# Kernel tuning notes

Hardware: AMD Instinct MI355X
Metric: run time of the kernel (lower is better)

Reference implementation:

```python
import jax, jax.numpy as jnp
import numpy as np

B, S, D, H = 2, 2048, 1024, 16
DH = D // H


def setup_inputs() -> dict:
    key = jax.random.key(0)
    ks = jax.random.split(key, 6)
    scale = 0.02
    X = jax.random.normal(ks[0], (B, S, D), dtype=jnp.float32)
    masks = jax.random.randint(ks[1], (B, S), 0, 2).astype(jnp.int32)
    Wq = jax.random.normal(ks[2], (D, D), dtype=jnp.float32) * scale
    Wk = jax.random.normal(ks[3], (D, D), dtype=jnp.float32) * scale
    Wv = jax.random.normal(ks[4], (D, D), dtype=jnp.float32) * scale
    Wo = jax.random.normal(ks[5], (D, D), dtype=jnp.float32) * scale
    return {"X": X, "masks": masks, "Wq": Wq, "Wk": Wk, "Wv": Wv, "Wo": Wo}


def reference(X, masks, Wq, Wk, Wv, Wo):
    b, s, d = X.shape
    masks_b = masks.astype(bool)                       # [B,S] key validity
    lookahead = jnp.triu(jnp.ones((s, s), dtype=bool), 1)  # [S,S] future positions
    pad = ~masks_b[:, None, :]                         # [B,1,S] -> invalid keys
    invalid = pad | lookahead[None, :, :]              # [B,S,S]
    valid = (~invalid)[:, None, :, :].astype(X.dtype)  # [B,1,S,S]

    def split_heads(Y):  # [B,S,D] -> [B,H,S,DH]
        return Y.reshape(b, s, H, DH).transpose(0, 2, 1, 3)

    Q = split_heads(X @ Wq.T)
    K = split_heads(X @ Wk.T)
    V = split_heads(X @ Wv.T)

    Qn = Q / jnp.sqrt(jnp.sum(Q * Q, axis=-1, keepdims=True))
    Kn = K / jnp.sqrt(jnp.sum(K * K, axis=-1, keepdims=True))

    scores = jnp.einsum('bhqd,bhkd->bhqk', Qn, Kn)     # cosine similarities
    att = jax.nn.relu(scores) * valid                  # relu + causal/pad mask
    ctx = jnp.einsum('bhqk,bhkd->bhqd', att, V)
    ctx = ctx * masks_b[:, None, :, None].astype(X.dtype)  # zero padded queries

    out = ctx.transpose(0, 2, 1, 3).reshape(b, s, d)
    return out @ Wo.T
```

## Files before the change

### kernel.cpp

```cpp
#include <hip/hip_runtime.h>
#include <hip/hip_bf16.h>

#define BB 2
#define SS 2048
#define DD 1024
#define HH 16
#define MMR (BB*SS)
#define ND3 3072

typedef __hip_bfloat16 bf;
typedef __bf16 bf16x8 __attribute__((ext_vector_type(8)));
typedef float f32x4 __attribute__((ext_vector_type(4)));
typedef float f32x16 __attribute__((ext_vector_type(16)));

#define VMCNT(n) asm volatile("s_waitcnt vmcnt(" #n ")" ::: "memory")

__device__ __forceinline__ f32x4 mfma16(bf16x8 a, bf16x8 b, f32x4 c) {
    return __builtin_amdgcn_mfma_f32_16x16x32_bf16(a, b, c, 0, 0, 0);
}
__device__ __forceinline__ f32x16 mfma32(bf16x8 a, bf16x8 b, f32x16 c) {
    return __builtin_amdgcn_mfma_f32_32x32x16_bf16(a, b, c, 0, 0, 0);
}
__device__ __forceinline__ unsigned cvt_pk_bf16(float lo, float hi) {
    unsigned r;
    asm("v_cvt_pk_bf16_f32 %0, %1, %2" : "=v"(r) : "v"(lo), "v"(hi));
    return r;
}
__device__ __forceinline__ void pl32swap(unsigned& a, unsigned& b) {
    asm("v_permlane32_swap_b32 %0, %1" : "+v"(a), "+v"(b));
}
__device__ __forceinline__ void glds16(const bf* g, bf* l) {
    __builtin_amdgcn_global_load_lds(
        (const __attribute__((address_space(1))) void*)g,
        (__attribute__((address_space(3))) void*)l,
        16, 0, 0);
}

__global__ __launch_bounds__(256) void k_convert(const float* __restrict__ X,
                                                 const float* __restrict__ Wq,
                                                 const float* __restrict__ Wk,
                                                 const float* __restrict__ Wv,
                                                 const float* __restrict__ Wo,
                                                 bf* __restrict__ Xb,
                                                 bf* __restrict__ Wqkv,
                                                 bf* __restrict__ Wob) {
    const int bid = blockIdx.x;
    const float* src;
    bf* dst;
    int off;
    if (bid < 4096) {
        src = X; dst = Xb; off = bid;
    } else {
        const int r = (bid - 4096) >> 10;
        src = (r == 0) ? Wq : (r == 1) ? Wk : (r == 2) ? Wv : Wo;
        dst = (r < 3) ? (Wqkv + (size_t)r * 1048576) : Wob;
        off = (bid - 4096) & 1023;
    }
    const int j = (off * 256 + threadIdx.x) * 4;
    float4 v = *(const float4*)(src + j);
    bf tmp[4];
    tmp[0] = __float2bfloat16(v.x);
    tmp[1] = __float2bfloat16(v.y);
    tmp[2] = __float2bfloat16(v.z);
    tmp[3] = __float2bfloat16(v.w);
    *(uint2*)(dst + j) = *(const uint2*)tmp;
}

__global__ __launch_bounds__(512, 6) void k_gemm8(const bf* __restrict__ A,
                                                  const bf* __restrict__ Bt,
                                                  const int* __restrict__ masks,
                                                  bf* __restrict__ Qn,
                                                  bf* __restrict__ Kn,
                                                  bf* __restrict__ Vt,
                                                  int nx, int K) {
    __shared__ __align__(16) bf Asm[3][128 * 32];
    __shared__ __align__(16) bf Bsm[3][128 * 32];
    const int tid = threadIdx.x;
    const int w = tid >> 6, lane = tid & 63, g = lane >> 4, rl = lane & 15;
    const int cpx = gridDim.x >> 3;
    const int swz = (blockIdx.x & 7) * cpx + (blockIdx.x >> 3);
    const int m0 = (swz / nx) * 128, n0 = (swz % nx) * 128;
    const int wr = (w >> 1) * 32, wc = (w & 1) * 64;
    const int lrow = lane >> 2, lseg = lane & 3;
    const int xseg = lseg ^ ((lrow >> 1) & 3);

    f32x4 acc[2][4] = {};
    const bf* Ap = A + (size_t)m0 * K;
    const bf* Bp = Bt + (size_t)n0 * K;

    auto stage = [&](int bi, int k0) {
        glds16(Ap + (size_t)(w * 16 + lrow) * K + k0 + xseg * 8, &Asm[bi][w * 512]);
        glds16(Bp + (size_t)(w * 16 + lrow) * K + k0 + xseg * 8, &Bsm[bi][w * 512]);
    };

    const int T = K >> 5;
    stage(0, 0);
    stage(1, 32);
    int cur = 0, nxt = 2;
    for (int t = 0; t < T; ++t) {
        __builtin_amdgcn_sched_barrier(0);
        if (t < T - 1) { VMCNT(2); } else { VMCNT(0); }
        __builtin_amdgcn_s_barrier();
        __builtin_amdgcn_sched_barrier(0);
        if (t + 2 < T) stage(nxt, (t + 2) * 32);

        const bf* Ab = Asm[cur];
        const bf* Bb = Bsm[cur];
        bf16x8 af[2], bfr[4];
#pragma unroll
        for (int m = 0; m < 2; ++m) {
            const int row = wr + m * 16 + rl;
            af[m] = __builtin_bit_cast(bf16x8,
                *(const int4*)&Ab[row * 32 + (g ^ ((row >> 1) & 3)) * 8]);
        }
#pragma unroll
        for (int n = 0; n < 4; ++n) {
            const int row = wc + n * 16 + rl;
            bfr[n] = __builtin_bit_cast(bf16x8,
                *(const int4*)&Bb[row * 32 + (g ^ ((row >> 1) & 3)) * 8]);
        }
        __builtin_amdgcn_s_setprio(1);
#pragma unroll
        for (int m = 0; m < 2; ++m)
#pragma unroll
            for (int n = 0; n < 4; ++n)
                acc[m][n] = mfma16(af[m], bfr[n], acc[m][n]);
        __builtin_amdgcn_s_setprio(0);

        cur = (cur == 2) ? 0 : cur + 1;
        nxt = (nxt == 2) ? 0 : nxt + 1;
    }

    const int ncol0 = n0 + wc;
    if (ncol0 < 2048) {
        bf* dst = (ncol0 < 1024) ? Qn : Kn;
        const int h2 = (ncol0 >> 6) & 15;
#pragma unroll
        for (int m = 0; m < 2; ++m) {
#pragma unroll
            for (int ri = 0; ri < 4; ++ri) {
                const int row = m0 + wr + m * 16 + g * 4 + ri;
                float ss = 0.f;
#pragma unroll
                for (int n = 0; n < 4; ++n) ss += acc[m][n][ri] * acc[m][n][ri];
#pragma unroll
                for (int d = 1; d < 16; d <<= 1) ss += __shfl_xor(ss, d, 64);
                const float sc = rsqrtf(ss) * (masks[row] ? 1.0f : 0.0f);
                const int b = row >> 11, s = row & 2047;
                const size_t base = ((size_t)(b * HH + h2) * SS + s) * 64;
#pragma unroll
                for (int n = 0; n < 4; ++n)
                    dst[base + n * 16 + rl] = __float2bfloat16(acc[m][n][ri] * sc);
            }
        }
    } else {
        const int h2 = (ncol0 - 2048) >> 6;
        const int b = (m0 + wr) >> 11;
        const int sb = ((m0 + wr) & 2047) + g * 4;
#pragma unroll
        for (int m = 0; m < 2; ++m)
#pragma unroll
            for (int n = 0; n < 4; ++n) {
                const int d = n * 16 + rl;
                bf t4[4];
#pragma unroll
                for (int ri = 0; ri < 4; ++ri) t4[ri] = __float2bfloat16(acc[m][n][ri]);
                *(uint2*)&Vt[((size_t)(b * HH + h2) * 64 + d) * SS + sb + m * 16] =
                    *(uint2*)t4;
            }
    }
}

__global__ __launch_bounds__(256) void k_gemm(const bf* __restrict__ A,
                                              const bf* __restrict__ Bt,
                                              float* __restrict__ Cf,
                                              int nx, int N, int K) {
    constexpr int BM = 64, BN = 128;
    __shared__ __align__(16) bf Asm[3][BM * 32];
    __shared__ __align__(16) bf Bsm[3][BN * 32];
    const int tid = threadIdx.x;
    const int w = tid >> 6, lane = tid & 63, g = lane >> 4, rl = lane & 15;
    const int cpx = gridDim.x >> 3;
    const int swz = (blockIdx.x & 7) * cpx + (blockIdx.x >> 3);
    const int m0 = (swz / nx) * BM, n0 = (swz % nx) * BN;
    const int wr = (w >> 1) * 32, wc = (w & 1) * 64;
    const int lrow = lane >> 2, lseg = lane & 3;
    const int xseg = lseg ^ ((lrow >> 1) & 3);

    f32x4 acc[2][4] = {};
    const bf* Ap = A + (size_t)m0 * K;
    const bf* Bp = Bt + (size_t)n0 * K;

    auto stage = [&](int bi, int k0) {
        glds16(Ap + (size_t)(w * 16 + lrow) * K + k0 + xseg * 8, &Asm[bi][w * 512]);
#pragma unroll
        for (int u = 0; u < 2; ++u)
            glds16(Bp + (size_t)(u * 64 + w * 16 + lrow) * K + k0 + xseg * 8,
                   &Bsm[bi][(u * 64 + w * 16) * 32]);
    };

    const int T = K >> 5;
    stage(0, 0);
    stage(1, 32);
    int cur = 0, nxt = 2;
    for (int t = 0; t < T; ++t) {
        __builtin_amdgcn_sched_barrier(0);
        if (t < T - 1) { VMCNT(3); } else { VMCNT(0); }
        __builtin_amdgcn_s_barrier();
        __builtin_amdgcn_sched_barrier(0);
        if (t + 2 < T) stage(nxt, (t + 2) * 32);

        const bf* Ab = Asm[cur];
        const bf* Bb = Bsm[cur];
        bf16x8 af[2], bfr[4];
#pragma unroll
        for (int m = 0; m < 2; ++m) {
            const int row = wr + m * 16 + rl;
            af[m] = __builtin_bit_cast(bf16x8,
                *(const int4*)&Ab[row * 32 + (g ^ ((row >> 1) & 3)) * 8]);
        }
#pragma unroll
        for (int n = 0; n < 4; ++n) {
            const int row = wc + n * 16 + rl;
            bfr[n] = __builtin_bit_cast(bf16x8,
                *(const int4*)&Bb[row * 32 + (g ^ ((row >> 1) & 3)) * 8]);
        }
        __builtin_amdgcn_s_setprio(1);
#pragma unroll
        for (int m = 0; m < 2; ++m)
#pragma unroll
            for (int n = 0; n < 4; ++n)
                acc[m][n] = mfma16(af[m], bfr[n], acc[m][n]);
        __builtin_amdgcn_s_setprio(0);

        cur = (cur == 2) ? 0 : cur + 1;
        nxt = (nxt == 2) ? 0 : nxt + 1;
    }

#pragma unroll
    for (int m = 0; m < 2; ++m)
#pragma unroll
        for (int n = 0; n < 4; ++n)
#pragma unroll
            for (int ri = 0; ri < 4; ++ri)
                Cf[(size_t)(m0 + wr + m * 16 + g * 4 + ri) * N + n0 + wc + n * 16 + rl] =
                    acc[m][n][ri];
}

__global__ __launch_bounds__(256) void k_attn(const bf* __restrict__ Qn,
                                              const bf* __restrict__ Kn,
                                              const bf* __restrict__ Vt,
                                              bf* __restrict__ Ctx) {
    __shared__ __align__(16) bf Ksm[2][64 * 64];
    __shared__ __align__(16) bf Vsm[2][64 * 64];

    const int idx = blockIdx.x;
    const int qt = 31 - (idx >> 5);
    const int by = idx & 31;
    const int b = by >> 4, h = by & 15;
    const int tid = threadIdx.x;
    const int w = tid >> 6, lane = tid & 63;
    const int l31 = lane & 31, hl = lane >> 5;
    const int qh = w >> 1;
    const int kp = w & 1;
    const int qw = qt * 64 + qh * 32;
    const int qg = qw + l31;

    const bf* Qp = Qn + (size_t)by * SS * 64;
    const bf* Kp = Kn + (size_t)by * SS * 64;
    const bf* Vp = Vt + (size_t)by * 64 * SS;

    bf16x8 aqs[4];
#pragma unroll
    for (int st = 0; st < 4; ++st)
        aqs[st] = __builtin_bit_cast(bf16x8,
            *(const int4*)(Qp + (size_t)(qw + l31) * 64 + st * 16 + hl * 8));

    const int srow = lane >> 3;
    const int sblk = (lane & 7) ^ srow;

    const bf* ksr = Kp + (size_t)(w * 16 + srow) * 64 + sblk * 8;
    const bf* vsr = Vp + (size_t)(w * 16 + srow) * SS + sblk * 8;
    bf* const kdst = &Ksm[0][w * 1024];
    bf* const vdst = &Vsm[0][w * 1024];

    auto stageP = [&](int buf, const bf* ks, const bf* vs) {
        glds16(ks,            kdst + buf * 4096);
        glds16(ks + 512,      kdst + buf * 4096 + 512);
        glds16(vs,            vdst + buf * 4096);
        glds16(vs + 8 * SS,   vdst + buf * 4096 + 512);
    };

    f32x16 accd[2] = {};

    auto doTile = [&](const bf* Ks, const bf* Vs, int t) {
        const int kb = t * 64 + kp * 32;
        if (kb > qw + 31) return;
        f32x16 pc = {};
        const int r = kp * 32 + l31;
#pragma unroll
        for (int st = 0; st < 4; ++st) {
            bf16x8 ak = __builtin_bit_cast(bf16x8,
                *(const int4*)&Ks[r * 64 + (((2 * st + hl) ^ (r & 7)) << 3)]);
            pc = mfma32(ak, aqs[st], pc);
        }
        const bool dg = (kb + 31 > qw);
        float pv[16];
#pragma unroll
        for (int m2 = 0; m2 < 16; ++m2) {
            float v = fmaxf(pc[m2], 0.0f);
            if (dg) {
                const int kg = kb + (m2 & 3) + 8 * (m2 >> 2) + 4 * hl;
                if (kg > qg) v = 0.0f;
            }
            pv[m2] = v;
        }
        unsigned P[8];
#pragma unroll
        for (int m2 = 0; m2 < 8; ++m2) P[m2] = cvt_pk_bf16(pv[2 * m2], pv[2 * m2 + 1]);
        pl32swap(P[0], P[2]);
        pl32swap(P[1], P[3]);
        pl32swap(P[4], P[6]);
        pl32swap(P[5], P[7]);
#pragma unroll
        for (int s = 0; s < 2; ++s) {
            uint4 pw = {P[4 * s + 0], P[4 * s + 1], P[4 * s + 2], P[4 * s + 3]};
            bf16x8 pa = __builtin_bit_cast(bf16x8, pw);
#pragma unroll
            for (int dt = 0; dt < 2; ++dt) {
                const int d = dt * 32 + l31;
                const int slot = kp * 4 + s * 2 + hl;
                bf16x8 bv = __builtin_bit_cast(bf16x8,
                    *(const int4*)&Vs[d * 64 + ((slot ^ (d & 7)) << 3)]);
                accd[dt] = mfma32(pa, bv, accd[dt]);
            }
        }
    };

    stageP(0, ksr, vsr);
    ksr += 4096; vsr += 64;
    __syncthreads();

    int t = 0;
    while (t + 1 <= qt) {
        stageP(1, ksr, vsr);
        ksr += 4096; vsr += 64;
        doTile(&Ksm[0][0], &Vsm[0][0], t);
        __syncthreads();
        if (t + 2 <= qt) {
            stageP(0, ksr, vsr);
            ksr += 4096; vsr += 64;
        }
        doTile(&Ksm[1][0], &Vsm[1][0], t + 1);
        __syncthreads();
        t += 2;
    }
    if (t <= qt) {
        doTile(&Ksm[0][0], &Vsm[0][0], t);
        __syncthreads();
    }

    float* red = (float*)&Ksm[0][0];
    if (kp == 1) {
#pragma unroll
        for (int dt = 0; dt < 2; ++dt)
#pragma unroll
            for (int m2 = 0; m2 < 16; ++m2)
                red[qh * 2048 + (dt * 16 + m2) * 64 + lane] = accd[dt][m2];
    }
    __syncthreads();
    if (kp == 0) {
#pragma unroll
        for (int dt = 0; dt < 2; ++dt)
#pragma unroll
            for (int m2 = 0; m2 < 16; ++m2) {
                const float v = accd[dt][m2] + red[qh * 2048 + (dt * 16 + m2) * 64 + lane];
                const int q = qw + (m2 & 3) + 8 * (m2 >> 2) + 4 * hl;
                const int d = dt * 32 + l31;
                Ctx[(size_t)(b * SS + q) * DD + h * 64 + d] = __float2bfloat16(v);
            }
    }
}

extern "C" void kernel_launch(void* const* d_in, const int* in_sizes, int n_in,
                              void* d_out, int out_size, void* d_ws, size_t ws_size,
                              hipStream_t stream) {
    const float* X  = (const float*)d_in[0];
    const int* masks = (const int*)d_in[1];
    const float* Wq = (const float*)d_in[2];
    const float* Wk = (const float*)d_in[3];
    const float* Wv = (const float*)d_in[4];
    const float* Wo = (const float*)d_in[5];
    float* out = (float*)d_out;
    char* ws = (char*)d_ws;

    const size_t MB = 1024 * 1024;
    bf* Xb   = (bf*)(ws);
    bf* Wqkv = (bf*)(ws + 8  * MB);
    bf* Wob  = (bf*)(ws + 14 * MB);
    bf* Qn   = (bf*)(ws + 16 * MB);
    bf* Kn   = (bf*)(ws + 24 * MB);
    bf* Vt   = (bf*)(ws + 32 * MB);
    bf* Ctx  = (bf*)(ws + 40 * MB);

    k_convert<<<8192, 256, 0, stream>>>(X, Wq, Wk, Wv, Wo, Xb, Wqkv, Wob);

    k_gemm8<<<(ND3 / 128) * (MMR / 128), 512, 0, stream>>>(
        Xb, Wqkv, masks, Qn, Kn, Vt, ND3 / 128, DD);

    k_attn<<<1024, 256, 0, stream>>>(Qn, Kn, Vt, Ctx);

    k_gemm<<<(DD / 128) * (MMR / 64), 256, 0, stream>>>(
        Ctx, Wob, out, DD / 128, DD, DD);
}
```

Measured before the change: 95.71 us.

## Switch QKV GEMM to double-buffered LDS with unrolled pingpong loop and higher occupancy

Replaces the triple-buffered LDS pipeline, which used explicit vmcnt waits, with a double buffer. The main loop is unrolled by two so buffer indices are compile-time constants, and source pointers are advanced incrementally. Launch bounds now ask for 8 waves per SIMD instead of 6, helped by the smaller LDS footprint. In exchange the prefetch distance shrinks to one tile, and each __syncthreads waits on all outstanding loads, which can expose global memory latency. The unroll also assumes T is even.

```diff
diff --git a/kernel.cpp b/kernel.cpp
--- a/kernel.cpp
+++ b/kernel.cpp
@@ -66,15 +66,15 @@
     *(uint2*)(dst + j) = *(const uint2*)tmp;
 }
 
-__global__ __launch_bounds__(512, 6) void k_gemm8(const bf* __restrict__ A,
+__global__ __launch_bounds__(512, 8) void k_gemm8(const bf* __restrict__ A,
                                                   const bf* __restrict__ Bt,
                                                   const int* __restrict__ masks,
                                                   bf* __restrict__ Qn,
                                                   bf* __restrict__ Kn,
                                                   bf* __restrict__ Vt,
                                                   int nx, int K) {
-    __shared__ __align__(16) bf Asm[3][128 * 32];
-    __shared__ __align__(16) bf Bsm[3][128 * 32];
+    __shared__ __align__(16) bf Asm[2][128 * 32];
+    __shared__ __align__(16) bf Bsm[2][128 * 32];
     const int tid = threadIdx.x;
     const int w = tid >> 6, lane = tid & 63, g = lane >> 4, rl = lane & 15;
     const int cpx = gridDim.x >> 3;
@@ -85,27 +85,19 @@
     const int xseg = lseg ^ ((lrow >> 1) & 3);
 
     f32x4 acc[2][4] = {};
-    const bf* Ap = A + (size_t)m0 * K;
-    const bf* Bp = Bt + (size_t)n0 * K;
-
-    auto stage = [&](int bi, int k0) {
-        glds16(Ap + (size_t)(w * 16 + lrow) * K + k0 + xseg * 8, &Asm[bi][w * 512]);
-        glds16(Bp + (size_t)(w * 16 + lrow) * K + k0 + xseg * 8, &Bsm[bi][w * 512]);
+
+    const bf* asr = A + (size_t)(m0 + w * 16 + lrow) * K + xseg * 8;
+    const bf* bsr = Bt + (size_t)(n0 + w * 16 + lrow) * K + xseg * 8;
+    bf* const adst = &Asm[0][w * 512];
+    bf* const bdst = &Bsm[0][w * 512];
+
+    auto stageP = [&](int buf) {
+        glds16(asr, adst + buf * 4096);
+        glds16(bsr, bdst + buf * 4096);
+        asr += 32; bsr += 32;
     };
 
-    const int T = K >> 5;
-    stage(0, 0);
-    stage(1, 32);
-    int cur = 0, nxt = 2;
-    for (int t = 0; t < T; ++t) {
-        __builtin_amdgcn_sched_barrier(0);
-        if (t < T - 1) { VMCNT(2); } else { VMCNT(0); }
-        __builtin_amdgcn_s_barrier();
-        __builtin_amdgcn_sched_barrier(0);
-        if (t + 2 < T) stage(nxt, (t + 2) * 32);
-
-        const bf* Ab = Asm[cur];
-        const bf* Bb = Bsm[cur];
+    auto computeT = [&](const bf* Ab, const bf* Bb) {
         bf16x8 af[2], bfr[4];
 #pragma unroll
         for (int m = 0; m < 2; ++m) {
@@ -126,9 +118,18 @@
             for (int n = 0; n < 4; ++n)
                 acc[m][n] = mfma16(af[m], bfr[n], acc[m][n]);
         __builtin_amdgcn_s_setprio(0);
-
-        cur = (cur == 2) ? 0 : cur + 1;
-        nxt = (nxt == 2) ? 0 : nxt + 1;
+    };
+
+    const int T = K >> 5;
+    stageP(0);
+    __syncthreads();
+    for (int t = 0; t < T; t += 2) {
+        stageP(1);
+        computeT(&Asm[0][0], &Bsm[0][0]);
+        __syncthreads();
+        if (t + 2 < T) stageP(0);
+        computeT(&Asm[1][0], &Bsm[1][0]);
+        __syncthreads();
     }
 
     const int ncol0 = n0 + wc;
```

Result: slower. 128.5 us (+34.2%).
